# Optimization experiments

Hardware: AMD Instinct MI355X
Metric: run time of the kernel (lower is better)

Reference implementation:

```python
import jax, jax.numpy as jnp
import numpy as np

HIDDEN = 1024
NUM_HEADS = 16
HEAD_DIM = HIDDEN // NUM_HEADS
ROPE_BASE = 10000.0


def _rope_cos_sin(seq_len, dtype):
    # inv_freq over even indices of head_dim
    inv_freq = 1.0 / (ROPE_BASE ** (jnp.arange(0, HEAD_DIM, 2, dtype=jnp.float32) / HEAD_DIM))
    t = jnp.arange(seq_len, dtype=jnp.float32)
    freqs = t[:, None] * inv_freq[None, :]            # (S, head_dim/2)
    emb = jnp.concatenate([freqs, freqs], axis=-1)    # (S, head_dim)
    cos = jnp.cos(emb)[None, None, :, :].astype(dtype)
    sin = jnp.sin(emb)[None, None, :, :].astype(dtype)
    return cos, sin


def _rotate_interleaved(x):
    # stack((-x[...,1::2], x[...,::2]), -1).flatten(-2) — interleaved pair rotation
    x1 = x[..., ::2]
    x2 = x[..., 1::2]
    return jnp.stack((-x2, x1), axis=-1).reshape(x.shape)


def _apply_rope(x, cos, sin):
    return x * cos + _rotate_interleaved(x) * sin


def setup_inputs() -> dict:
    key = jax.random.key(0)
    k0, k1, k2, k3, k4 = jax.random.split(key, 5)
    B, S = 2, 2048
    scale = 1.0 / np.sqrt(HIDDEN)
    return {
        "hidden_states": jax.random.normal(k0, (B, S, HIDDEN), dtype=jnp.float32),
        "Wq": jax.random.normal(k1, (HIDDEN, HIDDEN), dtype=jnp.float32) * scale,
        "Wk": jax.random.normal(k2, (HIDDEN, HIDDEN), dtype=jnp.float32) * scale,
        "Wv": jax.random.normal(k3, (HIDDEN, HIDDEN), dtype=jnp.float32) * scale,
        "Wo": jax.random.normal(k4, (HIDDEN, HIDDEN), dtype=jnp.float32) * scale,
    }


def reference(hidden_states, Wq, Wk, Wv, Wo):
    B, S, _ = hidden_states.shape
    # torch Linear: y = x @ W.T  (W is (out, in))
    def proj(x, W):
        y = jnp.einsum('bsd,ed->bse', x, W)
        return y.reshape(B, S, NUM_HEADS, HEAD_DIM).transpose(0, 2, 1, 3)  # (B,H,S,Dh)

    q = proj(hidden_states, Wq)
    k = proj(hidden_states, Wk)
    v = proj(hidden_states, Wv)

    cos, sin = _rope_cos_sin(S, hidden_states.dtype)
    q = _apply_rope(q, cos, sin)
    k = _apply_rope(k, cos, sin)

    scores = jnp.einsum('bhqd,bhkd->bhqk', q, k) / jnp.sqrt(jnp.asarray(HEAD_DIM, hidden_states.dtype))
    attn = jax.nn.softmax(scores, axis=-1)
    out = jnp.einsum('bhqk,bhkd->bhqd', attn, v)
    out = out.transpose(0, 2, 1, 3).reshape(B, S, HIDDEN)
    return jnp.einsum('bsd,ed->bse', out, Wo)
```

## Files before the change

kernel.cpp:

```cpp
#include <hip/hip_runtime.h>

typedef __attribute__((ext_vector_type(4)))  float  f32x4;
typedef __attribute__((ext_vector_type(16))) float  f32x16;
typedef __attribute__((ext_vector_type(8)))  short  s16x8;

__device__ __forceinline__ unsigned short f2bf(float f) {
    union { float f; unsigned u; } v; v.f = f;
    unsigned u = v.u + 0x7fffu + ((v.u >> 16) & 1u);
    return (unsigned short)(u >> 16);
}

__device__ __forceinline__ unsigned cvtpk(float lo, float hi_) {
    unsigned r;
    asm("v_cvt_pk_bf16_f32 %0, %1, %2" : "=v"(r) : "v"(lo), "v"(hi_));
    return r;
}

__device__ __forceinline__ float ex2(float x) {
#if __has_builtin(__builtin_amdgcn_exp2f)
    return __builtin_amdgcn_exp2f(x);
#else
    return exp2f(x);
#endif
}

__device__ __forceinline__ void gl_lds16(const unsigned short* g, unsigned short* l) {
    __builtin_amdgcn_global_load_lds(
        (const __attribute__((address_space(1))) void*)g,
        (__attribute__((address_space(3))) void*)l, 16, 0, 0);
}

__device__ __forceinline__ f32x4 mfma16(s16x8 a, s16x8 b, f32x4 c) {
    return __builtin_amdgcn_mfma_f32_16x16x32_bf16(a, b, c, 0, 0, 0);
}
__device__ __forceinline__ f32x16 mfma32(s16x8 a, s16x8 b, f32x16 c) {
    return __builtin_amdgcn_mfma_f32_32x32x16_bf16(a, b, c, 0, 0, 0);
}

__global__ __launch_bounds__(256) void k_prep(
    const float* __restrict__ X,  const float* __restrict__ Wq,
    const float* __restrict__ Wk, const float* __restrict__ Wv,
    const float* __restrict__ Wo,
    unsigned short* __restrict__ Xb,  unsigned short* __restrict__ Wqb,
    unsigned short* __restrict__ Wkb, unsigned short* __restrict__ Wvb,
    unsigned short* __restrict__ Wob,
    float* __restrict__ ct, float* __restrict__ st)
{
    int i = blockIdx.x * 256 + threadIdx.x;
    if (i < 2097152) {
        const float* s; unsigned short* d; int o;
        if (i < 1048576) { s = X; d = Xb; o = i; }
        else {
            int j = i - 1048576;
            int wsel = j >> 18; o = j & 262143;
            s = (wsel == 0) ? Wq : (wsel == 1) ? Wk : (wsel == 2) ? Wv : Wo;
            d = (wsel == 0) ? Wqb : (wsel == 1) ? Wkb : (wsel == 2) ? Wvb : Wob;
        }
        float4 f = reinterpret_cast<const float4*>(s)[o];
        ushort4 u;
        u.x = f2bf(f.x); u.y = f2bf(f.y); u.z = f2bf(f.z); u.w = f2bf(f.w);
        reinterpret_cast<ushort4*>(d)[o] = u;
    } else {
        int j = i - 2097152;
        int e0 = j << 2;
        int sq = e0 >> 6, d0 = e0 & 63;
        float4 cv, sv;
        #pragma unroll
        for (int k = 0; k < 4; k++) {
            int d = d0 + k;
            float invf = ex2(-(float)(d & 31) * 0.4152410118609203f);
            float ang = (float)sq * invf;
            float ss, cc;
            sincosf(ang, &ss, &cc);
            ((float*)&cv)[k] = cc; ((float*)&sv)[k] = ss;
        }
        *(float4*)&ct[e0] = cv;
        *(float4*)&st[e0] = sv;
    }
}

__global__ __launch_bounds__(256) void k_gemm_qkv(
    const unsigned short* __restrict__ Xb,
    const unsigned short* __restrict__ Wqb,
    const unsigned short* __restrict__ Wkb,
    const unsigned short* __restrict__ Wvb,
    const float* __restrict__ ct, const float* __restrict__ st,
    unsigned short* __restrict__ Qo, unsigned short* __restrict__ Ko,
    unsigned short* __restrict__ Vt)
{
    __shared__ __attribute__((aligned(16))) unsigned short As[2][128 * 32];
    __shared__ __attribute__((aligned(16))) unsigned short Bs[2][128 * 32];
    const int z = blockIdx.z;
    const int tid = threadIdx.x;
    const int lane = tid & 63;
    const int w  = tid >> 6;
    const int wm = (w >> 1) * 64, wn = (w & 1) * 64;
    const int r  = lane & 15, rg = lane >> 4;
    const int t8 = tid * 8;

    const unsigned short *Ap, *Bp;
    int m0, n0;
    if (z < 2) { Ap = Xb;  Bp = z ? Wkb : Wqb; m0 = blockIdx.x * 128; n0 = blockIdx.y * 128; }
    else       { Ap = Wvb; Bp = Xb;            m0 = blockIdx.y * 128; n0 = blockIdx.x * 128; }

    f32x4 acc[4][4];
    const f32x4 zf = {0.f, 0.f, 0.f, 0.f};
    #pragma unroll
    for (int i = 0; i < 4; i++)
        #pragma unroll
        for (int j = 0; j < 4; j++) acc[i][j] = zf;

    const unsigned short* ga = Ap + (size_t)(m0 + (tid >> 2)) * 1024 + (tid & 3) * 8;
    const unsigned short* gb = Bp + (size_t)(n0 + (tid >> 2)) * 1024 + (tid & 3) * 8;

    gl_lds16(ga,             &As[0][t8]);
    gl_lds16(ga + 64 * 1024, &As[0][2048 + t8]);
    gl_lds16(gb,             &Bs[0][t8]);
    gl_lds16(gb + 64 * 1024, &Bs[0][2048 + t8]);
    asm volatile("s_waitcnt vmcnt(0)" ::: "memory");
    __syncthreads();

    int cur = 0;
    for (int k = 0; k < 32; ++k) {
        if (k < 31) {
            int k0 = (k + 1) * 32;
            gl_lds16(ga + k0,             &As[cur ^ 1][t8]);
            gl_lds16(ga + k0 + 64 * 1024, &As[cur ^ 1][2048 + t8]);
            gl_lds16(gb + k0,             &Bs[cur ^ 1][t8]);
            gl_lds16(gb + k0 + 64 * 1024, &Bs[cur ^ 1][2048 + t8]);
        }
        s16x8 af[4], bfr[4];
        #pragma unroll
        for (int mi = 0; mi < 4; mi++) af[mi]  = *(const s16x8*)&As[cur][(wm + mi * 16 + r) * 32 + rg * 8];
        #pragma unroll
        for (int ni = 0; ni < 4; ni++) bfr[ni] = *(const s16x8*)&Bs[cur][(wn + ni * 16 + r) * 32 + rg * 8];
        __builtin_amdgcn_s_setprio(1);
        #pragma unroll
        for (int mi = 0; mi < 4; mi++)
            #pragma unroll
            for (int ni = 0; ni < 4; ni++)
                acc[mi][ni] = mfma16(af[mi], bfr[ni], acc[mi][ni]);
        __builtin_amdgcn_s_setprio(0);
        __syncthreads();
        cur ^= 1;
    }

    if (z < 2) {
        unsigned short* Out = z ? Ko : Qo;
        const float qscale = z ? 1.0f : 0.18033688011112042f;
        #pragma unroll
        for (int mi = 0; mi < 4; mi++)
            #pragma unroll
            for (int ni = 0; ni < 4; ni++)
                #pragma unroll
                for (int rr = 0; rr < 4; rr++) {
                    float v = acc[mi][ni][rr];
                    float vp = __shfl_xor(v, 1);
                    int m = m0 + wm + mi * 16 + rg * 4 + rr;
                    int e = n0 + wn + ni * 16 + r;
                    int s = m & 2047, d = e & 63;
                    float c = ct[(s << 6) + d], sn = st[(s << 6) + d];
                    float sgn = (e & 1) ? 1.0f : -1.0f;
                    v = fmaf(v, c, sgn * vp * sn) * qscale;
                    int b = m >> 11, h = e >> 6;
                    Out[(((size_t)(b * 16 + h) * 2048 + s) << 6) + d] = f2bf(v);
                }
    } else {
        #pragma unroll
        for (int mi = 0; mi < 4; mi++)
            #pragma unroll
            for (int ni = 0; ni < 4; ni++)
                #pragma unroll
                for (int rr = 0; rr < 4; rr++) {
                    int e  = m0 + wm + mi * 16 + rg * 4 + rr;
                    int mm = n0 + wn + ni * 16 + r;
                    int b = mm >> 11, s = mm & 2047, h = e >> 6, d = e & 63;
                    Vt[((size_t)(b * 16 + h) * 64 + d) * 2048 + s] = f2bf(acc[mi][ni][rr]);
                }
    }
}

__global__ __launch_bounds__(128, 3) void k_attn(
    const unsigned short* __restrict__ Q,
    const unsigned short* __restrict__ K,
    const unsigned short* __restrict__ Vt,
    unsigned short* __restrict__ AO)
{
    __shared__ __attribute__((aligned(16))) unsigned short Ks[2][64 * 64];
    __shared__ __attribute__((aligned(16))) unsigned short Vs[2][64 * 64];
    const int bh = blockIdx.y;
    const int q0 = blockIdx.x * 64;
    const int tid = threadIdx.x, lane = tid & 63, w = tid >> 6;
    const int ln31 = lane & 31, hi = lane >> 5;
    const int swz = (ln31 & 7) << 3;
    const unsigned short* Qp = Q  + (size_t)bh * 2048 * 64;
    const unsigned short* Kp = K  + (size_t)bh * 2048 * 64;
    const unsigned short* Vp = Vt + (size_t)bh * 64 * 2048;

    s16x8 qf[4];
    #pragma unroll
    for (int ds = 0; ds < 4; ds++)
        qf[ds] = *(const s16x8*)&Qp[(size_t)(q0 + w * 32 + ln31) * 64 + ds * 16 + hi * 8];

    f32x16 o0, o1;
    #pragma unroll
    for (int r = 0; r < 16; r++) { o0[r] = 0.f; o1[r] = 0.f; }
    float mrun = -1e30f, lrun = 0.f;

    int sr[4], sc[4], tt8[4];
    #pragma unroll
    for (int j = 0; j < 4; j++) {
        int c = tid + j * 128;
        sr[j] = c >> 3;
        sc[j] = ((c & 7) * 8) ^ ((sr[j] & 7) << 3);
        tt8[j] = c * 8;
    }
    const unsigned short *gk[4], *gv[4];
    #pragma unroll
    for (int j = 0; j < 4; j++) {
        gk[j] = Kp + (size_t)sr[j] * 64   + sc[j];
        gv[j] = Vp + (size_t)sr[j] * 2048 + sc[j];
    }

    #pragma unroll
    for (int j = 0; j < 4; j++) gl_lds16(gk[j], &Ks[0][tt8[j]]);
    #pragma unroll
    for (int j = 0; j < 4; j++) gl_lds16(gv[j], &Vs[0][tt8[j]]);
    asm volatile("s_waitcnt vmcnt(0)" ::: "memory");
    __syncthreads();

    int cur = 0;
    for (int t = 0; t < 32; ++t) {
        if (t < 31) {
            size_t ok = (size_t)(t + 1) * 4096;
            size_t ov = (size_t)(t + 1) * 64;
            #pragma unroll
            for (int j = 0; j < 4; j++) gl_lds16(gk[j] + ok, &Ks[cur ^ 1][tt8[j]]);
            #pragma unroll
            for (int j = 0; j < 4; j++) gl_lds16(gv[j] + ov, &Vs[cur ^ 1][tt8[j]]);
        }
        const unsigned short* Kb = Ks[cur];
        const unsigned short* Vb = Vs[cur];

        f32x16 s0, s1;
        #pragma unroll
        for (int r = 0; r < 16; r++) { s0[r] = 0.f; s1[r] = 0.f; }
        __builtin_amdgcn_s_setprio(1);
        #pragma unroll
        for (int ds = 0; ds < 4; ds++) {
            s16x8 k0 = *(const s16x8*)&Kb[ ln31       * 64 + ((ds * 16 + hi * 8) ^ swz)];
            s16x8 k1 = *(const s16x8*)&Kb[(32 + ln31) * 64 + ((ds * 16 + hi * 8) ^ swz)];
            s0 = mfma32(k0, qf[ds], s0);
            s1 = mfma32(k1, qf[ds], s1);
        }
        __builtin_amdgcn_s_setprio(0);

        float tm = -1e30f;
        #pragma unroll
        for (int r = 0; r < 16; r++) tm = fmaxf(tm, fmaxf(s0[r], s1[r]));
        tm = fmaxf(tm, __shfl_xor(tm, 32));
        if (!__all(tm <= mrun + 8.0f)) {
            float mnew = fmaxf(mrun, tm);
            float al = ex2(mrun - mnew);
            mrun = mnew;
            lrun *= al;
            #pragma unroll
            for (int r = 0; r < 16; r++) { o0[r] *= al; o1[r] *= al; }
        }
        float rs = 0.f;
        #pragma unroll
        for (int r = 0; r < 16; r++) { float p = ex2(s0[r] - mrun); s0[r] = p; rs += p; }
        #pragma unroll
        for (int r = 0; r < 16; r++) { float p = ex2(s1[r] - mrun); s1[r] = p; rs += p; }
        rs += __shfl_xor(rs, 32);
        lrun += rs;

        s16x8 pa[4];
        #pragma unroll
        for (int ks = 0; ks < 4; ks++) {
            float x0, x1, x2, x3, x4, x5, x6, x7;
            if      (ks == 0) { x0=s0[0]; x1=s0[1]; x2=s0[2];  x3=s0[3];  x4=s0[4];  x5=s0[5];  x6=s0[6];  x7=s0[7];  }
            else if (ks == 1) { x0=s0[8]; x1=s0[9]; x2=s0[10]; x3=s0[11]; x4=s0[12]; x5=s0[13]; x6=s0[14]; x7=s0[15]; }
            else if (ks == 2) { x0=s1[0]; x1=s1[1]; x2=s1[2];  x3=s1[3];  x4=s1[4];  x5=s1[5];  x6=s1[6];  x7=s1[7];  }
            else              { x0=s1[8]; x1=s1[9]; x2=s1[10]; x3=s1[11]; x4=s1[12]; x5=s1[13]; x6=s1[14]; x7=s1[15]; }
            unsigned a  = cvtpk(x0, x1);
            unsigned a2 = cvtpk(x2, x3);
            unsigned b  = cvtpk(x4, x5);
            unsigned b2 = cvtpk(x6, x7);
            asm volatile("v_permlane32_swap_b32 %0, %1" : "+v"(a),  "+v"(b));
            asm volatile("v_permlane32_swap_b32 %0, %1" : "+v"(a2), "+v"(b2));
            union { s16x8 v; unsigned u[4]; } pu;
            pu.u[0] = a; pu.u[1] = a2; pu.u[2] = b; pu.u[3] = b2;
            pa[ks] = pu.v;
        }

        __builtin_amdgcn_s_setprio(1);
        #pragma unroll
        for (int ks = 0; ks < 4; ks++) {
            s16x8 v0 = *(const s16x8*)&Vb[ ln31       * 64 + ((ks * 16 + hi * 8) ^ swz)];
            s16x8 v1 = *(const s16x8*)&Vb[(32 + ln31) * 64 + ((ks * 16 + hi * 8) ^ swz)];
            o0 = mfma32(v0, pa[ks], o0);
            o1 = mfma32(v1, pa[ks], o1);
        }
        __builtin_amdgcn_s_setprio(0);

        __syncthreads();
        cur ^= 1;
    }

    float inv = 1.0f / lrun;
    const int b = bh >> 4, h = bh & 15;
    const int qg = q0 + w * 32 + ln31;
    size_t base = ((size_t)(b * 2048 + qg)) * 1024 + h * 64;
    #pragma unroll
    for (int dc = 0; dc < 2; dc++) {
        #pragma unroll
        for (int g = 0; g < 4; g++) {
            float y0, y1, y2, y3;
            if (dc == 0) { y0 = o0[4*g]; y1 = o0[4*g+1]; y2 = o0[4*g+2]; y3 = o0[4*g+3]; }
            else         { y0 = o1[4*g]; y1 = o1[4*g+1]; y2 = o1[4*g+2]; y3 = o1[4*g+3]; }
            unsigned lo  = cvtpk(y0 * inv, y1 * inv);
            unsigned hi2 = cvtpk(y2 * inv, y3 * inv);
            int d = dc * 32 + 8 * g + 4 * hi;
            uint2 stv; stv.x = lo; stv.y = hi2;
            *(uint2*)&AO[base + d] = stv;
        }
    }
}

__global__ __launch_bounds__(256) void k_gemm_out(
    const unsigned short* __restrict__ AOb,
    const unsigned short* __restrict__ Wob,
    float* __restrict__ Out)
{
    __shared__ __attribute__((aligned(16))) unsigned short As[2][128 * 32];
    __shared__ __attribute__((aligned(16))) unsigned short Bs[2][128 * 32];
    const int tid = threadIdx.x;
    const int lane = tid & 63;
    const int w  = tid >> 6;
    const int wm = (w >> 1) * 64, wn = (w & 1) * 64;
    const int r  = lane & 15, rg = lane >> 4;
    const int m0 = blockIdx.x * 128, n0 = blockIdx.y * 128;
    const int t8 = tid * 8;

    f32x4 acc[4][4];
    const f32x4 zf = {0.f, 0.f, 0.f, 0.f};
    #pragma unroll
    for (int i = 0; i < 4; i++)
        #pragma unroll
        for (int j = 0; j < 4; j++) acc[i][j] = zf;

    const unsigned short* ga = AOb + (size_t)(m0 + (tid >> 2)) * 1024 + (tid & 3) * 8;
    const unsigned short* gb = Wob + (size_t)(n0 + (tid >> 2)) * 1024 + (tid & 3) * 8;

    gl_lds16(ga,             &As[0][t8]);
    gl_lds16(ga + 64 * 1024, &As[0][2048 + t8]);
    gl_lds16(gb,             &Bs[0][t8]);
    gl_lds16(gb + 64 * 1024, &Bs[0][2048 + t8]);
    asm volatile("s_waitcnt vmcnt(0)" ::: "memory");
    __syncthreads();

    int cur = 0;
    for (int k = 0; k < 32; ++k) {
        if (k < 31) {
            int k0 = (k + 1) * 32;
            gl_lds16(ga + k0,             &As[cur ^ 1][t8]);
            gl_lds16(ga + k0 + 64 * 1024, &As[cur ^ 1][2048 + t8]);
            gl_lds16(gb + k0,             &Bs[cur ^ 1][t8]);
            gl_lds16(gb + k0 + 64 * 1024, &Bs[cur ^ 1][2048 + t8]);
        }
        s16x8 af[4], bfr[4];
        #pragma unroll
        for (int mi = 0; mi < 4; mi++) af[mi]  = *(const s16x8*)&As[cur][(wm + mi * 16 + r) * 32 + rg * 8];
        #pragma unroll
        for (int ni = 0; ni < 4; ni++) bfr[ni] = *(const s16x8*)&Bs[cur][(wn + ni * 16 + r) * 32 + rg * 8];
        __builtin_amdgcn_s_setprio(1);
        #pragma unroll
        for (int mi = 0; mi < 4; mi++)
            #pragma unroll
            for (int ni = 0; ni < 4; ni++)
                acc[mi][ni] = mfma16(af[mi], bfr[ni], acc[mi][ni]);
        __builtin_amdgcn_s_setprio(0);
        __syncthreads();
        cur ^= 1;
    }

    #pragma unroll
    for (int mi = 0; mi < 4; mi++)
        #pragma unroll
        for (int ni = 0; ni < 4; ni++)
            #pragma unroll
            for (int rr = 0; rr < 4; rr++) {
                int m = m0 + wm + mi * 16 + rg * 4 + rr;
                int e = n0 + wn + ni * 16 + r;
                Out[(size_t)m * 1024 + e] = acc[mi][ni][rr];
            }
}

extern "C" void kernel_launch(void* const* d_in, const int* in_sizes, int n_in,
                              void* d_out, int out_size, void* d_ws, size_t ws_size,
                              hipStream_t stream) {
    const float* X  = (const float*)d_in[0];
    const float* Wq = (const float*)d_in[1];
    const float* Wk = (const float*)d_in[2];
    const float* Wv = (const float*)d_in[3];
    const float* Wo = (const float*)d_in[4];
    float* Out = (float*)d_out;
    char* ws = (char*)d_ws;

    unsigned short* Xb   = (unsigned short*)(ws);
    unsigned short* Wqb  = (unsigned short*)(ws + 8388608);
    unsigned short* Wkb  = (unsigned short*)(ws + 10485760);
    unsigned short* Wvb  = (unsigned short*)(ws + 12582912);
    unsigned short* Wob  = (unsigned short*)(ws + 14680064);
    unsigned short* Qb   = (unsigned short*)(ws + 16777216);
    unsigned short* Kb   = (unsigned short*)(ws + 25165824);
    unsigned short* Vtb  = (unsigned short*)(ws + 33554432);
    unsigned short* AOb  = (unsigned short*)(ws + 41943040);
    float*          cosT = (float*)(ws + 50331648);
    float*          sinT = (float*)(ws + 50855936);

    k_prep<<<8320, 256, 0, stream>>>(X, Wq, Wk, Wv, Wo, Xb, Wqb, Wkb, Wvb, Wob, cosT, sinT);
    k_gemm_qkv<<<dim3(32, 8, 3), 256, 0, stream>>>(Xb, Wqb, Wkb, Wvb, cosT, sinT, Qb, Kb, Vtb);
    k_attn<<<dim3(32, 32), 128, 0, stream>>>(Qb, Kb, Vtb, AOb);
    k_gemm_out<<<dim3(32, 8), 256, 0, stream>>>(AOb, Wob, Out);
}
```

Before: 234.8 us.

## Widen attention blocks to 128 queries, shrink output GEMM tile, grid-stride prep

The attention kernel now runs 4 waves per block covering 128 query rows, so each K/V tile staged in shared memory is reused by twice as many queries, with half as many loads per thread. The output projection GEMM uses 64x128 tiles instead of 128x128, launching 512 blocks so more CUs are busy on this small problem. The prep kernel becomes grid-stride with 2048 blocks to cut block launch overhead. The trade-offs are fewer attention blocks (512), which may lower occupancy, and less register reuse per wave in the smaller GEMM tile.

```diff
diff --git a/kernel.cpp b/kernel.cpp
--- a/kernel.cpp
+++ b/kernel.cpp
@@ -46,36 +46,37 @@
     unsigned short* __restrict__ Wob,
     float* __restrict__ ct, float* __restrict__ st)
 {
-    int i = blockIdx.x * 256 + threadIdx.x;
-    if (i < 2097152) {
-        const float* s; unsigned short* d; int o;
-        if (i < 1048576) { s = X; d = Xb; o = i; }
-        else {
-            int j = i - 1048576;
-            int wsel = j >> 18; o = j & 262143;
-            s = (wsel == 0) ? Wq : (wsel == 1) ? Wk : (wsel == 2) ? Wv : Wo;
-            d = (wsel == 0) ? Wqb : (wsel == 1) ? Wkb : (wsel == 2) ? Wvb : Wob;
-        }
-        float4 f = reinterpret_cast<const float4*>(s)[o];
-        ushort4 u;
-        u.x = f2bf(f.x); u.y = f2bf(f.y); u.z = f2bf(f.z); u.w = f2bf(f.w);
-        reinterpret_cast<ushort4*>(d)[o] = u;
-    } else {
-        int j = i - 2097152;
-        int e0 = j << 2;
-        int sq = e0 >> 6, d0 = e0 & 63;
-        float4 cv, sv;
-        #pragma unroll
-        for (int k = 0; k < 4; k++) {
-            int d = d0 + k;
-            float invf = ex2(-(float)(d & 31) * 0.4152410118609203f);
-            float ang = (float)sq * invf;
-            float ss, cc;
-            sincosf(ang, &ss, &cc);
-            ((float*)&cv)[k] = cc; ((float*)&sv)[k] = ss;
-        }
-        *(float4*)&ct[e0] = cv;
-        *(float4*)&st[e0] = sv;
+    for (int i = blockIdx.x * 256 + threadIdx.x; i < 2129920; i += 2048 * 256) {
+        if (i < 2097152) {
+            const float* s; unsigned short* d; int o;
+            if (i < 1048576) { s = X; d = Xb; o = i; }
+            else {
+                int j = i - 1048576;
+                int wsel = j >> 18; o = j & 262143;
+                s = (wsel == 0) ? Wq : (wsel == 1) ? Wk : (wsel == 2) ? Wv : Wo;
+                d = (wsel == 0) ? Wqb : (wsel == 1) ? Wkb : (wsel == 2) ? Wvb : Wob;
+            }
+            float4 f = reinterpret_cast<const float4*>(s)[o];
+            ushort4 u;
+            u.x = f2bf(f.x); u.y = f2bf(f.y); u.z = f2bf(f.z); u.w = f2bf(f.w);
+            reinterpret_cast<ushort4*>(d)[o] = u;
+        } else {
+            int j = i - 2097152;
+            int e0 = j << 2;
+            int sq = e0 >> 6, d0 = e0 & 63;
+            float4 cv, sv;
+            #pragma unroll
+            for (int k = 0; k < 4; k++) {
+                int d = d0 + k;
+                float invf = ex2(-(float)(d & 31) * 0.4152410118609203f);
+                float ang = (float)sq * invf;
+                float ss, cc;
+                sincosf(ang, &ss, &cc);
+                ((float*)&cv)[k] = cc; ((float*)&sv)[k] = ss;
+            }
+            *(float4*)&ct[e0] = cv;
+            *(float4*)&st[e0] = sv;
+        }
     }
 }
 
@@ -180,7 +181,7 @@
     }
 }
 
-__global__ __launch_bounds__(128, 3) void k_attn(
+__global__ __launch_bounds__(256, 3) void k_attn(
     const unsigned short* __restrict__ Q,
     const unsigned short* __restrict__ K,
     const unsigned short* __restrict__ Vt,
@@ -189,7 +190,7 @@
     __shared__ __attribute__((aligned(16))) unsigned short Ks[2][64 * 64];
     __shared__ __attribute__((aligned(16))) unsigned short Vs[2][64 * 64];
     const int bh = blockIdx.y;
-    const int q0 = blockIdx.x * 64;
+    const int q0 = blockIdx.x * 128;
     const int tid = threadIdx.x, lane = tid & 63, w = tid >> 6;
     const int ln31 = lane & 31, hi = lane >> 5;
     const int swz = (ln31 & 7) << 3;
@@ -207,25 +208,19 @@
     for (int r = 0; r < 16; r++) { o0[r] = 0.f; o1[r] = 0.f; }
     float mrun = -1e30f, lrun = 0.f;
 
-    int sr[4], sc[4], tt8[4];
-    #pragma unroll
-    for (int j = 0; j < 4; j++) {
-        int c = tid + j * 128;
-        sr[j] = c >> 3;
-        sc[j] = ((c & 7) * 8) ^ ((sr[j] & 7) << 3);
-        tt8[j] = c * 8;
-    }
-    const unsigned short *gk[4], *gv[4];
-    #pragma unroll
-    for (int j = 0; j < 4; j++) {
-        gk[j] = Kp + (size_t)sr[j] * 64   + sc[j];
-        gv[j] = Vp + (size_t)sr[j] * 2048 + sc[j];
-    }
-
-    #pragma unroll
-    for (int j = 0; j < 4; j++) gl_lds16(gk[j], &Ks[0][tt8[j]]);
-    #pragma unroll
-    for (int j = 0; j < 4; j++) gl_lds16(gv[j], &Vs[0][tt8[j]]);
+    const int c1 = tid + 256;
+    const int sr0 = tid >> 3, sc0 = ((tid & 7) * 8) ^ ((sr0 & 7) << 3);
+    const int sr1 = c1 >> 3,  sc1 = ((c1 & 7) * 8) ^ ((sr1 & 7) << 3);
+    const unsigned short* gk0 = Kp + (size_t)sr0 * 64   + sc0;
+    const unsigned short* gk1 = Kp + (size_t)sr1 * 64   + sc1;
+    const unsigned short* gv0 = Vp + (size_t)sr0 * 2048 + sc0;
+    const unsigned short* gv1 = Vp + (size_t)sr1 * 2048 + sc1;
+    const int t80 = tid * 8, t81 = c1 * 8;
+
+    gl_lds16(gk0, &Ks[0][t80]);
+    gl_lds16(gk1, &Ks[0][t81]);
+    gl_lds16(gv0, &Vs[0][t80]);
+    gl_lds16(gv1, &Vs[0][t81]);
     asm volatile("s_waitcnt vmcnt(0)" ::: "memory");
     __syncthreads();
 
@@ -234,10 +229,10 @@
         if (t < 31) {
             size_t ok = (size_t)(t + 1) * 4096;
             size_t ov = (size_t)(t + 1) * 64;
-            #pragma unroll
-            for (int j = 0; j < 4; j++) gl_lds16(gk[j] + ok, &Ks[cur ^ 1][tt8[j]]);
-            #pragma unroll
-            for (int j = 0; j < 4; j++) gl_lds16(gv[j] + ov, &Vs[cur ^ 1][tt8[j]]);
+            gl_lds16(gk0 + ok, &Ks[cur ^ 1][t80]);
+            gl_lds16(gk1 + ok, &Ks[cur ^ 1][t81]);
+            gl_lds16(gv0 + ov, &Vs[cur ^ 1][t80]);
+            gl_lds16(gv1 + ov, &Vs[cur ^ 1][t81]);
         }
         const unsigned short* Kb = Ks[cur];
         const unsigned short* Vb = Vs[cur];
@@ -333,28 +328,24 @@
     const unsigned short* __restrict__ Wob,
     float* __restrict__ Out)
 {
-    __shared__ __attribute__((aligned(16))) unsigned short As[2][128 * 32];
+    __shared__ __attribute__((aligned(16))) unsigned short As[2][64 * 32];
     __shared__ __attribute__((aligned(16))) unsigned short Bs[2][128 * 32];
     const int tid = threadIdx.x;
     const int lane = tid & 63;
     const int w  = tid >> 6;
-    const int wm = (w >> 1) * 64, wn = (w & 1) * 64;
     const int r  = lane & 15, rg = lane >> 4;
-    const int m0 = blockIdx.x * 128, n0 = blockIdx.y * 128;
+    const int m0 = blockIdx.x * 64, n0 = blockIdx.y * 128;
     const int t8 = tid * 8;
 
-    f32x4 acc[4][4];
+    f32x4 acc[4][2];
     const f32x4 zf = {0.f, 0.f, 0.f, 0.f};
     #pragma unroll
-    for (int i = 0; i < 4; i++)
-        #pragma unroll
-        for (int j = 0; j < 4; j++) acc[i][j] = zf;
+    for (int i = 0; i < 4; i++) { acc[i][0] = zf; acc[i][1] = zf; }
 
     const unsigned short* ga = AOb + (size_t)(m0 + (tid >> 2)) * 1024 + (tid & 3) * 8;
     const unsigned short* gb = Wob + (size_t)(n0 + (tid >> 2)) * 1024 + (tid & 3) * 8;
 
     gl_lds16(ga,             &As[0][t8]);
-    gl_lds16(ga + 64 * 1024, &As[0][2048 + t8]);
     gl_lds16(gb,             &Bs[0][t8]);
     gl_lds16(gb + 64 * 1024, &Bs[0][2048 + t8]);
     asm volatile("s_waitcnt vmcnt(0)" ::: "memory");
@@ -365,20 +356,19 @@
         if (k < 31) {
             int k0 = (k + 1) * 32;
             gl_lds16(ga + k0,             &As[cur ^ 1][t8]);
-            gl_lds16(ga + k0 + 64 * 1024, &As[cur ^ 1][2048 + t8]);
             gl_lds16(gb + k0,             &Bs[cur ^ 1][t8]);
             gl_lds16(gb + k0 + 64 * 1024, &Bs[cur ^ 1][2048 + t8]);
         }
-        s16x8 af[4], bfr[4];
-        #pragma unroll
-        for (int mi = 0; mi < 4; mi++) af[mi]  = *(const s16x8*)&As[cur][(wm + mi * 16 + r) * 32 + rg * 8];
-        #pragma unroll
-        for (int ni = 0; ni < 4; ni++) bfr[ni] = *(const s16x8*)&Bs[cur][(wn + ni * 16 + r) * 32 + rg * 8];
+        s16x8 af[4], bfr[2];
+        #pragma unroll
+        for (int mi = 0; mi < 4; mi++) af[mi]  = *(const s16x8*)&As[cur][(mi * 16 + r) * 32 + rg * 8];
+        #pragma unroll
+        for (int ni = 0; ni < 2; ni++) bfr[ni] = *(const s16x8*)&Bs[cur][(w * 32 + ni * 16 + r) * 32 + rg * 8];
         __builtin_amdgcn_s_setprio(1);
         #pragma unroll
         for (int mi = 0; mi < 4; mi++)
             #pragma unroll
-            for (int ni = 0; ni < 4; ni++)
+            for (int ni = 0; ni < 2; ni++)
                 acc[mi][ni] = mfma16(af[mi], bfr[ni], acc[mi][ni]);
         __builtin_amdgcn_s_setprio(0);
         __syncthreads();
@@ -388,11 +378,11 @@
     #pragma unroll
     for (int mi = 0; mi < 4; mi++)
         #pragma unroll
-        for (int ni = 0; ni < 4; ni++)
+        for (int ni = 0; ni < 2; ni++)
             #pragma unroll
             for (int rr = 0; rr < 4; rr++) {
-                int m = m0 + wm + mi * 16 + rg * 4 + rr;
-                int e = n0 + wn + ni * 16 + r;
+                int m = m0 + mi * 16 + rg * 4 + rr;
+                int e = n0 + w * 32 + ni * 16 + r;
                 Out[(size_t)m * 1024 + e] = acc[mi][ni][rr];
             }
 }
@@ -420,8 +410,8 @@
     float*          cosT = (float*)(ws + 50331648);
     float*          sinT = (float*)(ws + 50855936);
 
-    k_prep<<<8320, 256, 0, stream>>>(X, Wq, Wk, Wv, Wo, Xb, Wqb, Wkb, Wvb, Wob, cosT, sinT);
+    k_prep<<<2048, 256, 0, stream>>>(X, Wq, Wk, Wv, Wo, Xb, Wqb, Wkb, Wvb, Wob, cosT, sinT);
     k_gemm_qkv<<<dim3(32, 8, 3), 256, 0, stream>>>(Xb, Wqb, Wkb, Wvb, cosT, sinT, Qb, Kb, Vtb);
-    k_attn<<<dim3(32, 32), 128, 0, stream>>>(Qb, Kb, Vtb, AOb);
-    k_gemm_out<<<dim3(32, 8), 256, 0, stream>>>(AOb, Wob, Out);
-}
+    k_attn<<<dim3(16, 32), 256, 0, stream>>>(Qb, Kb, Vtb, AOb);
+    k_gemm_out<<<dim3(64, 8), 256, 0, stream>>>(AOb, Wob, Out);
+}
```

New measurement: 217.7 us. 1.08x faster.
